# Kernel tuning notes

Measured on AMD Instinct MI355X. Metric: run time of the kernel, lower is better.

## Reference

```python
import jax, jax.numpy as jnp
import numpy as np
from jax import lax

NPOINT = 1024
RADIUS = 0.2
NSAMPLE = 32
BN_EPS = 1e-5


def setup_inputs() -> dict:
    key = jax.random.key(0)
    ks = jax.random.split(key, 8)
    B, N, C = 16, 4096, 6
    xyz = jax.random.uniform(ks[0], (B, N, 3), jnp.float32)
    points = jax.random.normal(ks[1], (B, N, C), jnp.float32)
    dims = [3 + C, 64, 64, 128]
    inp = {"xyz": xyz, "points": points}
    for i in range(3):
        inp[f"W{i}"] = (jax.random.normal(ks[2 + i], (dims[i + 1], dims[i]), jnp.float32)
                         / np.sqrt(dims[i]).astype(np.float32))
        inp[f"b{i}"] = jnp.zeros((dims[i + 1],), jnp.float32)
        inp[f"g{i}"] = jnp.ones((dims[i + 1],), jnp.float32)
        inp[f"bb{i}"] = jnp.zeros((dims[i + 1],), jnp.float32)
    return inp


def _square_distance(a, b):
    # a: (B,S,3), b: (B,N,3) -> (B,S,N) squared euclidean distances
    return (jnp.sum(a * a, -1)[:, :, None]
            - 2.0 * jnp.einsum("bsd,bnd->bsn", a, b)
            + jnp.sum(b * b, -1)[:, None, :])


def _farthest_point_sample(xyz, npoint):
    # xyz: (B,N,3) -> (B,npoint) int32 indices. Deterministic init at index 0.
    B, N, _ = xyz.shape
    bidx = jnp.arange(B)

    def step(carry, _):
        dist, farthest = carry  # (B,N), (B,)
        centroid = xyz[bidx, farthest]  # (B,3)
        d = jnp.sum((xyz - centroid[:, None, :]) ** 2, -1)  # (B,N)
        dist = jnp.minimum(dist, d)
        nxt = jnp.argmax(dist, axis=-1).astype(jnp.int32)
        return (dist, nxt), farthest

    init = (jnp.full((B, N), 1e10, jnp.float32), jnp.zeros((B,), jnp.int32))
    _, idx = lax.scan(step, init, None, length=npoint)
    return idx.T  # (B, npoint)


def _ball_query(radius, nsample, xyz, new_xyz):
    # xyz: (B,N,3), new_xyz: (B,S,3) -> (B,S,nsample) int32 indices
    B, N, _ = xyz.shape
    S = new_xyz.shape[1]
    sqr = _square_distance(new_xyz, xyz)  # (B,S,N)
    group_idx = jnp.broadcast_to(jnp.arange(N, dtype=jnp.int32), (B, S, N))
    group_idx = jnp.where(sqr > radius * radius, N, group_idx)
    group_idx = jnp.sort(group_idx, axis=-1)[:, :, :nsample]
    first = group_idx[:, :, :1]
    return jnp.where(group_idx == N, first, group_idx)


def _index_points(points, idx):
    # points: (B,N,C), idx: (B,...) -> (B,...,C)
    return jax.vmap(lambda p, i: p[i])(points, idx)


def _mlp_bn_relu(x, params):
    # x: (..., Cin); BatchNorm1d in training mode over all flattened rows.
    shape = x.shape
    h = x.reshape(-1, shape[-1])
    for (W, b, g, bb) in params:
        h = h @ W.T + b
        mu = jnp.mean(h, axis=0)
        var = jnp.mean((h - mu) ** 2, axis=0)  # biased var (torch BN forward)
        h = (h - mu) * lax.rsqrt(var + BN_EPS) * g + bb
        h = jax.nn.relu(h)
    return h.reshape(*shape[:-1], -1)


def reference(xyz, points, W0, b0, g0, bb0, W1, b1, g1, bb1, W2, b2, g2, bb2):
    params = [(W0, b0, g0, bb0), (W1, b1, g1, bb1), (W2, b2, g2, bb2)]
    fps_idx = _farthest_point_sample(xyz, NPOINT)          # (B,S)
    new_xyz = _index_points(xyz, fps_idx)                  # (B,S,3)
    idx = _ball_query(RADIUS, NSAMPLE, xyz, new_xyz)       # (B,S,K)
    grouped_xyz = _index_points(xyz, idx) - new_xyz[:, :, None, :]  # (B,S,K,3)
    grouped_pts = _index_points(points, idx)               # (B,S,K,C)
    combined = jnp.concatenate([grouped_xyz, grouped_pts], axis=-1)
    out = _mlp_bn_relu(combined, params)                   # (B,S,K,128)
    new_points = jnp.max(out, axis=2)                      # (B,S,128)
    return new_xyz, new_points
```

## Files before the change

kernel.cpp:

```cpp
#include <hip/hip_runtime.h>

typedef unsigned short u16;
typedef unsigned long long u64;
typedef float f32x2 __attribute__((ext_vector_type(2)));

#define NN 4096
#define SS 1024
#define NSAMP 32
#define NGRP 16384
#define ROWS 524288
#define BN_EPS_F 1e-5f
#define INV_ROWS (1.0f/524288.0f)

__device__ __forceinline__ f32x2 pk_fma_sv(f32x2 w, f32x2 x, f32x2 c){
    f32x2 d; asm("v_pk_fma_f32 %0, %1, %2, %3" : "=v"(d) : "s"(w), "v"(x), "v"(c)); return d;
}

#define FPS_DPP_STEP(CTRL)                                                              \
    {   int hs = __builtin_amdgcn_update_dpp((int)(bk >> 32), (int)(bk >> 32),          \
                                             CTRL, 0xf, 0xf, false);                    \
        int ls = __builtin_amdgcn_update_dpp((int)bk, (int)bk, CTRL, 0xf, 0xf, false);  \
        u64 o = ((u64)(unsigned int)hs << 32) | (unsigned int)ls;                       \
        bk = bk > o ? bk : o; }

__global__ __launch_bounds__(256, 1) void fps_kernel(const float* __restrict__ xyz,
                                                     float* __restrict__ out,
                                                     float* __restrict__ stats){
    __shared__ float xs[NN], ys[NN], zs[NN];
    __shared__ u64 red[2][4];
    const int b = blockIdx.x;
    const int tid = threadIdx.x;
    if (b == 0){ stats[tid] = 0.0f; stats[tid + 256] = 0.0f; }
    const float* xb = xyz + (size_t)b * NN * 3;
    float px[16], py[16], pz[16], dreg[16];
    unsigned int inv[16];
    #pragma unroll
    for (int p = 0; p < 16; ++p){
        int i = tid + p * 256;
        float x = xb[i*3+0], y = xb[i*3+1], z = xb[i*3+2];
        px[p] = x; py[p] = y; pz[p] = z;
        xs[i] = x; ys[i] = y; zs[i] = z;
        dreg[p] = 1e10f;
        inv[p] = (unsigned int)(NN - 1 - i);
    }
    int cur = 0;
    __syncthreads();
    if (tid == 0){
        float* of = out + (size_t)b * SS * 3;
        of[0] = xs[0]; of[1] = ys[0]; of[2] = zs[0];
    }
    const int wave = tid >> 6, lane = tid & 63;
    for (int it = 1; it < SS; ++it){
        float cx = xs[cur], cy = ys[cur], cz = zs[cur];
        u64 t[16];
        #pragma unroll
        for (int p = 0; p < 16; ++p){
            float dx = __fsub_rn(px[p], cx);
            float dy = __fsub_rn(py[p], cy);
            float dz = __fsub_rn(pz[p], cz);
            float dd = __fadd_rn(__fadd_rn(__fmul_rn(dx,dx), __fmul_rn(dy,dy)),
                                 __fmul_rn(dz,dz));
            dreg[p] = fminf(dreg[p], dd);
            t[p] = ((u64)__float_as_uint(dreg[p]) << 32) | inv[p];
        }
        #pragma unroll
        for (int s = 8; s >= 1; s >>= 1)
            #pragma unroll
            for (int i2 = 0; i2 < s; ++i2)
                if (t[i2 + s] > t[i2]) t[i2] = t[i2 + s];
        u64 bk = t[0];
        FPS_DPP_STEP(0x111)
        FPS_DPP_STEP(0x112)
        FPS_DPP_STEP(0x114)
        FPS_DPP_STEP(0x118)
        FPS_DPP_STEP(0x142)
        FPS_DPP_STEP(0x143)
        unsigned int wh = (unsigned int)__builtin_amdgcn_readlane((int)(bk >> 32), 63);
        unsigned int wl = (unsigned int)__builtin_amdgcn_readlane((int)bk, 63);
        if (lane == 0) red[it & 1][wave] = ((u64)wh << 32) | wl;
        __syncthreads();
        u64 r0 = red[it & 1][0], r1 = red[it & 1][1];
        u64 r2 = red[it & 1][2], r3 = red[it & 1][3];
        u64 a01 = r0 > r1 ? r0 : r1;
        u64 a23 = r2 > r3 ? r2 : r3;
        u64 m0  = a01 > a23 ? a01 : a23;
        cur = (NN - 1 - (int)(m0 & 0xffffffffu)) & (NN - 1);
        if (tid == 0){
            float* of = out + ((size_t)b * SS + it) * 3;
            of[0] = xs[cur]; of[1] = ys[cur]; of[2] = zs[cur];
        }
    }
}

__global__ __launch_bounds__(256) void ballq_kernel(const float* __restrict__ xyz,
                                                    const float* __restrict__ outc,
                                                    u16* __restrict__ gidx){
    const int g = (blockIdx.x << 2) + (threadIdx.x >> 6);
    const int lane = threadIdx.x & 63;
    const int b = g >> 10;
    const float rr = 0.04f;
    const float* c = outc + (size_t)g * 3;
    float cx = c[0], cy = c[1], cz = c[2];
    float sa = __fadd_rn(__fadd_rn(__fmul_rn(cx,cx), __fmul_rn(cy,cy)), __fmul_rn(cz,cz));
    const float* xb = xyz + (size_t)b * NN * 3;
    u16* outp = gidx + (size_t)g * NSAMP;
    int count = 0, first = -1;
    const u64 below = (1ull << lane) - 1ull;
    for (int base = 0; base < NN && count < NSAMP; base += 512){
        u64 masks[8];
        #pragma unroll
        for (int u = 0; u < 8; ++u){
            int n = base + u * 64 + lane;
            float x = xb[n*3+0], y = xb[n*3+1], z = xb[n*3+2];
            float sb = __fadd_rn(__fadd_rn(__fmul_rn(x,x), __fmul_rn(y,y)), __fmul_rn(z,z));
            float dt = __fadd_rn(__fadd_rn(__fmul_rn(cx,x), __fmul_rn(cy,y)), __fmul_rn(cz,z));
            float sq = __fadd_rn(__fsub_rn(sa, __fmul_rn(2.0f, dt)), sb);
            masks[u] = __ballot(!(sq > rr));
        }
        #pragma unroll
        for (int u = 0; u < 8; ++u){
            u64 m = masks[u];
            bool w = (m >> lane) & 1ull;
            int pos = __popcll(m & below);
            if (w && (count + pos) < NSAMP) outp[count + pos] = (u16)(base + u * 64 + lane);
            if (first < 0 && m != 0ull) first = base + u * 64 + (__ffsll((long long)m) - 1);
            count += __popcll(m);
        }
    }
    for (int j = count + lane; j < NSAMP; j += 64) outp[j] = (u16)first;
}

__device__ __forceinline__ void gather_row(const float* __restrict__ xyz, const float* __restrict__ pts,
                                           const float* __restrict__ outc, const u16* __restrict__ gidx,
                                           int row, float* x){
    int g = row >> 5;
    int b = row >> 15;
    int i = gidx[row];
    const float* cc = outc + (size_t)g * 3;
    const float* xp = xyz + ((size_t)b * NN + i) * 3;
    const float* pp = pts + ((size_t)b * NN + i) * 6;
    x[0] = __fsub_rn(xp[0], cc[0]);
    x[1] = __fsub_rn(xp[1], cc[1]);
    x[2] = __fsub_rn(xp[2], cc[2]);
    #pragma unroll
    for (int k = 0; k < 6; ++k) x[3+k] = pp[k];
}

__device__ __forceinline__ void bn_coef(const float* sums, const float* ssqs,
                                        const float* g, const float* bbv, int ch,
                                        float* sc, float* sh){
    float mu = sums[ch] * INV_ROWS;
    float var = fmaf(-mu, mu, ssqs[ch] * INV_ROWS);
    var = fmaxf(var, 0.0f);
    float is = rsqrtf(var + BN_EPS_F);
    float s = is * g[ch];
    sc[ch] = s;
    sh[ch] = fmaf(-mu, s, bbv[ch]);
}

__global__ __launch_bounds__(256, 1) void stats1_kernel(const float* __restrict__ xyz, const float* __restrict__ pts,
                                                        const float* __restrict__ outc, const u16* __restrict__ gidx,
                                                        const float* __restrict__ W0f, const float* __restrict__ b0f,
                                                        float* __restrict__ stats){
    __shared__ float tr[256 * 65];
    __shared__ float accs[4][64], accq[4][64];
    const int row = blockIdx.x * 256 + threadIdx.x;
    float x[9];
    gather_row(xyz, pts, outc, gidx, row, x);
    #pragma unroll
    for (int j = 0; j < 64; ++j){
        float acc = b0f[j];
        #pragma unroll
        for (int k = 0; k < 9; ++k) acc = fmaf(x[k], W0f[j*9+k], acc);
        tr[threadIdx.x * 65 + j] = acc;
    }
    __syncthreads();
    const int ch = threadIdx.x & 63, qq = threadIdx.x >> 6;
    float s = 0.f, q = 0.f;
    for (int r = 0; r < 64; ++r){
        float v = tr[(qq * 64 + r) * 65 + ch];
        s += v; q = fmaf(v, v, q);
    }
    accs[qq][ch] = s; accq[qq][ch] = q;
    __syncthreads();
    if (threadIdx.x < 64){
        int c = threadIdx.x;
        atomicAdd(&stats[c], (accs[0][c] + accs[1][c]) + (accs[2][c] + accs[3][c]));
    } else if (threadIdx.x < 128){
        int c = threadIdx.x - 64;
        atomicAdd(&stats[64 + c], (accq[0][c] + accq[1][c]) + (accq[2][c] + accq[3][c]));
    }
}

__global__ __launch_bounds__(256, 1) void stats2_kernel(const float* __restrict__ xyz, const float* __restrict__ pts,
                                                        const float* __restrict__ outc, const u16* __restrict__ gidx,
                                                        const float* __restrict__ W0f, const float* __restrict__ b0f,
                                                        const float* __restrict__ W1f, const float* __restrict__ b1f,
                                                        const float* __restrict__ g0, const float* __restrict__ bb0,
                                                        float* __restrict__ stats){
    __shared__ float sc1[64], sh1[64];
    __shared__ float tr[256 * 65];
    __shared__ float accs[4][64], accq[4][64];
    if (threadIdx.x < 64) bn_coef(stats + 0, stats + 64, g0, bb0, threadIdx.x, sc1, sh1);
    __syncthreads();
    const int row = blockIdx.x * 256 + threadIdx.x;
    float x[9];
    gather_row(xyz, pts, outc, gidx, row, x);
    f32x2 x2p[32];
    #pragma unroll
    for (int j = 0; j < 64; ++j){
        float acc = b0f[j];
        #pragma unroll
        for (int k = 0; k < 9; ++k) acc = fmaf(x[k], W0f[j*9+k], acc);
        float v = fmaxf(fmaf(acc, sc1[j], sh1[j]), 0.f);
        if (j & 1) x2p[j >> 1].y = v; else x2p[j >> 1].x = v;
    }
    for (int ch = 0; ch < 64; ++ch){
        const f32x2* wp = (const f32x2*)(W1f + ch * 64);
        f32x2 A; A.x = b1f[ch]; A.y = 0.f;
        f32x2 B; B.x = 0.f;     B.y = 0.f;
        #pragma unroll
        for (int k2 = 0; k2 < 32; k2 += 2){
            A = pk_fma_sv(wp[k2],     x2p[k2],     A);
            B = pk_fma_sv(wp[k2 + 1], x2p[k2 + 1], B);
        }
        tr[threadIdx.x * 65 + ch] = (A.x + A.y) + (B.x + B.y);
    }
    __syncthreads();
    const int ch = threadIdx.x & 63, qq = threadIdx.x >> 6;
    float s = 0.f, q = 0.f;
    for (int r = 0; r < 64; ++r){
        float v = tr[(qq * 64 + r) * 65 + ch];
        s += v; q = fmaf(v, v, q);
    }
    accs[qq][ch] = s; accq[qq][ch] = q;
    __syncthreads();
    if (threadIdx.x < 64){
        int c = threadIdx.x;
        atomicAdd(&stats[128 + c], (accs[0][c] + accs[1][c]) + (accs[2][c] + accs[3][c]));
    } else if (threadIdx.x < 128){
        int c = threadIdx.x - 64;
        atomicAdd(&stats[192 + c], (accq[0][c] + accq[1][c]) + (accq[2][c] + accq[3][c]));
    }
}

__global__ __launch_bounds__(256, 1) void stats3_kernel(const float* __restrict__ xyz, const float* __restrict__ pts,
                                                        const float* __restrict__ outc, const u16* __restrict__ gidx,
                                                        const float* __restrict__ W0f, const float* __restrict__ b0f,
                                                        const float* __restrict__ W1f, const float* __restrict__ b1f,
                                                        const float* __restrict__ W2f, const float* __restrict__ b2f,
                                                        const float* __restrict__ g0, const float* __restrict__ bb0,
                                                        const float* __restrict__ g1, const float* __restrict__ bb1,
                                                        float* __restrict__ stats,
                                                        float* __restrict__ pmax, float* __restrict__ pmin){
    __shared__ float sc1[64], sh1[64], sc2[64], sh2[64];
    __shared__ float tr[256 * 65];
    __shared__ float accs[4][64], accq[4][64];
    if (threadIdx.x < 64){
        bn_coef(stats + 0,   stats + 64,  g0, bb0, threadIdx.x, sc1, sh1);
        bn_coef(stats + 128, stats + 192, g1, bb1, threadIdx.x, sc2, sh2);
    }
    __syncthreads();
    const int row = blockIdx.x * 256 + threadIdx.x;
    float x[9];
    gather_row(xyz, pts, outc, gidx, row, x);
    f32x2 x2p[32];
    #pragma unroll
    for (int j = 0; j < 64; ++j){
        float acc = b0f[j];
        #pragma unroll
        for (int k = 0; k < 9; ++k) acc = fmaf(x[k], W0f[j*9+k], acc);
        float v = fmaxf(fmaf(acc, sc1[j], sh1[j]), 0.f);
        if (j & 1) x2p[j >> 1].y = v; else x2p[j >> 1].x = v;
    }
    #pragma unroll
    for (int j = 0; j < 64; ++j){
        const f32x2* wp = (const f32x2*)(W1f + j * 64);
        f32x2 A; A.x = b1f[j]; A.y = 0.f;
        f32x2 B; B.x = 0.f;    B.y = 0.f;
        #pragma unroll
        for (int k2 = 0; k2 < 32; k2 += 2){
            A = pk_fma_sv(wp[k2],     x2p[k2],     A);
            B = pk_fma_sv(wp[k2 + 1], x2p[k2 + 1], B);
        }
        tr[threadIdx.x * 65 + j] = fmaxf(fmaf((A.x + A.y) + (B.x + B.y), sc2[j], sh2[j]), 0.f);
    }
    asm volatile("" ::: "memory");
    f32x2 x3p[32];
    #pragma unroll
    for (int j = 0; j < 32; ++j){
        x3p[j].x = tr[threadIdx.x * 65 + 2*j];
        x3p[j].y = tr[threadIdx.x * 65 + 2*j + 1];
    }
    const int ch = threadIdx.x & 63, qq = threadIdx.x >> 6;
    for (int half = 0; half < 2; ++half){
        for (int c64 = 0; c64 < 64; ++c64){
            int c = half * 64 + c64;
            const f32x2* wp = (const f32x2*)(W2f + c * 64);
            f32x2 A; A.x = b2f[c]; A.y = 0.f;
            f32x2 B; B.x = 0.f;    B.y = 0.f;
            #pragma unroll
            for (int k2 = 0; k2 < 32; k2 += 2){
                A = pk_fma_sv(wp[k2],     x3p[k2],     A);
                B = pk_fma_sv(wp[k2 + 1], x3p[k2 + 1], B);
            }
            tr[threadIdx.x * 65 + c64] = (A.x + A.y) + (B.x + B.y);
        }
        __syncthreads();
        float s = 0.f, q = 0.f;
        float mxA = -1e30f, mnA = 1e30f, mxB = -1e30f, mnB = 1e30f;
        for (int r = 0; r < 32; ++r){
            float v = tr[(qq * 64 + r) * 65 + ch];
            s += v; q = fmaf(v, v, q);
            mxA = fmaxf(mxA, v); mnA = fminf(mnA, v);
        }
        for (int r = 32; r < 64; ++r){
            float v = tr[(qq * 64 + r) * 65 + ch];
            s += v; q = fmaf(v, v, q);
            mxB = fmaxf(mxB, v); mnB = fminf(mnB, v);
        }
        int c = half * 64 + ch;
        int gA = blockIdx.x * 8 + 2 * qq;
        pmax[(size_t)gA * 128 + c] = mxA;
        pmin[(size_t)gA * 128 + c] = mnA;
        pmax[(size_t)(gA + 1) * 128 + c] = mxB;
        pmin[(size_t)(gA + 1) * 128 + c] = mnB;
        accs[qq][ch] = s; accq[qq][ch] = q;
        __syncthreads();
        if (threadIdx.x < 64){
            int cc = half * 64 + threadIdx.x;
            atomicAdd(&stats[256 + cc], (accs[0][threadIdx.x] + accs[1][threadIdx.x])
                                      + (accs[2][threadIdx.x] + accs[3][threadIdx.x]));
        } else if (threadIdx.x < 128){
            int t = threadIdx.x - 64;
            int cc = half * 64 + t;
            atomicAdd(&stats[384 + cc], (accq[0][t] + accq[1][t]) + (accq[2][t] + accq[3][t]));
        }
        __syncthreads();
    }
}

__global__ __launch_bounds__(256) void pool_kernel(const float* __restrict__ stats,
                                                   const float* __restrict__ g2, const float* __restrict__ bb2,
                                                   const float* __restrict__ pmax, const float* __restrict__ pmin,
                                                   float* __restrict__ out){
    __shared__ float sc[128], sh[128];
    if (threadIdx.x < 128) bn_coef(stats + 256, stats + 384, g2, bb2, threadIdx.x, sc, sh);
    __syncthreads();
    int o = blockIdx.x * 256 + threadIdx.x;
    int ch = o & 127;
    float a = fmaf(pmax[o], sc[ch], sh[ch]);
    float b = fmaf(pmin[o], sc[ch], sh[ch]);
    out[NGRP * 3 + o] = fmaxf(fmaxf(a, b), 0.0f);
}

extern "C" void kernel_launch(void* const* d_in, const int* in_sizes, int n_in,
                              void* d_out, int out_size, void* d_ws, size_t ws_size,
                              hipStream_t stream){
    const float* xyz = (const float*)d_in[0];
    const float* pts = (const float*)d_in[1];
    const float* W0  = (const float*)d_in[2];
    const float* b0  = (const float*)d_in[3];
    const float* g0  = (const float*)d_in[4];
    const float* bb0 = (const float*)d_in[5];
    const float* W1  = (const float*)d_in[6];
    const float* b1  = (const float*)d_in[7];
    const float* g1  = (const float*)d_in[8];
    const float* bb1 = (const float*)d_in[9];
    const float* W2  = (const float*)d_in[10];
    const float* b2  = (const float*)d_in[11];
    const float* g2  = (const float*)d_in[12];
    const float* bb2 = (const float*)d_in[13];
    float* out = (float*)d_out;

    if (ws_size < 17827840u) return;
    char*  ws    = (char*)d_ws;
    float* stats = (float*)ws;
    u16*   gidx  = (u16*)  (ws + 2048);
    float* pmax  = (float*)(ws + 1050624);
    float* pmin  = (float*)(ws + 9439232);

    fps_kernel  <<<16, 256, 0, stream>>>(xyz, out, stats);
    ballq_kernel<<<NGRP/4, 256, 0, stream>>>(xyz, out, gidx);
    stats1_kernel<<<ROWS/256, 256, 0, stream>>>(xyz, pts, out, gidx, W0, b0, stats);
    stats2_kernel<<<ROWS/256, 256, 0, stream>>>(xyz, pts, out, gidx, W0, b0, W1, b1, g0, bb0, stats);
    stats3_kernel<<<ROWS/256, 256, 0, stream>>>(xyz, pts, out, gidx, W0, b0, W1, b1, W2, b2,
                                                g0, bb0, g1, bb1, stats, pmax, pmin);
    pool_kernel <<<NGRP*128/256, 256, 0, stream>>>(stats, g2, bb2, pmax, pmin, out);
}
```

Measured before the change: 1.235 ms.

## Halve shared transpose buffer to 32 columns to allow four blocks per CU

The three BN-statistics kernels now stage 32 channels at a time in a 256x33 shared transpose buffer instead of all 64 in a 256x65 buffer, doing the reduction in two or four passes. Launch bounds go from one to four blocks per CU. This cuts LDS use per block from about 66KB to about 34KB and caps register use, so more waves can hide gather and ALU latency. The cost is extra barriers and reduction passes, more atomics per block, and a risk of register spills under the tighter launch bound, since stats3 keeps 64 f32x2 activation registers live.

```diff
diff --git a/kernel.cpp b/kernel.cpp
--- a/kernel.cpp
+++ b/kernel.cpp
@@ -158,49 +158,59 @@
     sh[ch] = fmaf(-mu, s, bbv[ch]);
 }
 
-__global__ __launch_bounds__(256, 1) void stats1_kernel(const float* __restrict__ xyz, const float* __restrict__ pts,
+
+__global__ __launch_bounds__(256, 4) void stats1_kernel(const float* __restrict__ xyz, const float* __restrict__ pts,
                                                         const float* __restrict__ outc, const u16* __restrict__ gidx,
                                                         const float* __restrict__ W0f, const float* __restrict__ b0f,
                                                         float* __restrict__ stats){
-    __shared__ float tr[256 * 65];
-    __shared__ float accs[4][64], accq[4][64];
+    __shared__ float tr[256 * 33];
+    __shared__ float accs[8][32], accq[8][32];
     const int row = blockIdx.x * 256 + threadIdx.x;
     float x[9];
     gather_row(xyz, pts, outc, gidx, row, x);
-    #pragma unroll
-    for (int j = 0; j < 64; ++j){
-        float acc = b0f[j];
-        #pragma unroll
-        for (int k = 0; k < 9; ++k) acc = fmaf(x[k], W0f[j*9+k], acc);
-        tr[threadIdx.x * 65 + j] = acc;
-    }
-    __syncthreads();
-    const int ch = threadIdx.x & 63, qq = threadIdx.x >> 6;
-    float s = 0.f, q = 0.f;
-    for (int r = 0; r < 64; ++r){
-        float v = tr[(qq * 64 + r) * 65 + ch];
-        s += v; q = fmaf(v, v, q);
-    }
-    accs[qq][ch] = s; accq[qq][ch] = q;
-    __syncthreads();
-    if (threadIdx.x < 64){
-        int c = threadIdx.x;
-        atomicAdd(&stats[c], (accs[0][c] + accs[1][c]) + (accs[2][c] + accs[3][c]));
-    } else if (threadIdx.x < 128){
-        int c = threadIdx.x - 64;
-        atomicAdd(&stats[64 + c], (accq[0][c] + accq[1][c]) + (accq[2][c] + accq[3][c]));
-    }
-}
-
-__global__ __launch_bounds__(256, 1) void stats2_kernel(const float* __restrict__ xyz, const float* __restrict__ pts,
+    const int ch = threadIdx.x & 31, oc = threadIdx.x >> 5;
+    #pragma unroll
+    for (int h2 = 0; h2 < 2; ++h2){
+        #pragma unroll
+        for (int j = 0; j < 32; ++j){
+            int jj = h2 * 32 + j;
+            float acc = b0f[jj];
+            #pragma unroll
+            for (int k = 0; k < 9; ++k) acc = fmaf(x[k], W0f[jj*9+k], acc);
+            tr[threadIdx.x * 33 + j] = acc;
+        }
+        __syncthreads();
+        float s = 0.f, q = 0.f;
+        for (int r = 0; r < 32; ++r){
+            float v = tr[(oc * 32 + r) * 33 + ch];
+            s += v; q = fmaf(v, v, q);
+        }
+        accs[oc][ch] = s; accq[oc][ch] = q;
+        __syncthreads();
+        if (threadIdx.x < 32){
+            int t = threadIdx.x;
+            float t0 = (accs[0][t] + accs[1][t]) + (accs[2][t] + accs[3][t]);
+            float t1 = (accs[4][t] + accs[5][t]) + (accs[6][t] + accs[7][t]);
+            atomicAdd(&stats[h2 * 32 + t], t0 + t1);
+        } else if (threadIdx.x < 64){
+            int t = threadIdx.x - 32;
+            float t0 = (accq[0][t] + accq[1][t]) + (accq[2][t] + accq[3][t]);
+            float t1 = (accq[4][t] + accq[5][t]) + (accq[6][t] + accq[7][t]);
+            atomicAdd(&stats[64 + h2 * 32 + t], t0 + t1);
+        }
+        __syncthreads();
+    }
+}
+
+__global__ __launch_bounds__(256, 4) void stats2_kernel(const float* __restrict__ xyz, const float* __restrict__ pts,
                                                         const float* __restrict__ outc, const u16* __restrict__ gidx,
                                                         const float* __restrict__ W0f, const float* __restrict__ b0f,
                                                         const float* __restrict__ W1f, const float* __restrict__ b1f,
                                                         const float* __restrict__ g0, const float* __restrict__ bb0,
                                                         float* __restrict__ stats){
     __shared__ float sc1[64], sh1[64];
-    __shared__ float tr[256 * 65];
-    __shared__ float accs[4][64], accq[4][64];
+    __shared__ float tr[256 * 33];
+    __shared__ float accs[8][32], accq[8][32];
     if (threadIdx.x < 64) bn_coef(stats + 0, stats + 64, g0, bb0, threadIdx.x, sc1, sh1);
     __syncthreads();
     const int row = blockIdx.x * 256 + threadIdx.x;
@@ -215,36 +225,45 @@
         float v = fmaxf(fmaf(acc, sc1[j], sh1[j]), 0.f);
         if (j & 1) x2p[j >> 1].y = v; else x2p[j >> 1].x = v;
     }
-    for (int ch = 0; ch < 64; ++ch){
-        const f32x2* wp = (const f32x2*)(W1f + ch * 64);
-        f32x2 A; A.x = b1f[ch]; A.y = 0.f;
-        f32x2 B; B.x = 0.f;     B.y = 0.f;
-        #pragma unroll
-        for (int k2 = 0; k2 < 32; k2 += 2){
-            A = pk_fma_sv(wp[k2],     x2p[k2],     A);
-            B = pk_fma_sv(wp[k2 + 1], x2p[k2 + 1], B);
-        }
-        tr[threadIdx.x * 65 + ch] = (A.x + A.y) + (B.x + B.y);
-    }
-    __syncthreads();
-    const int ch = threadIdx.x & 63, qq = threadIdx.x >> 6;
-    float s = 0.f, q = 0.f;
-    for (int r = 0; r < 64; ++r){
-        float v = tr[(qq * 64 + r) * 65 + ch];
-        s += v; q = fmaf(v, v, q);
-    }
-    accs[qq][ch] = s; accq[qq][ch] = q;
-    __syncthreads();
-    if (threadIdx.x < 64){
-        int c = threadIdx.x;
-        atomicAdd(&stats[128 + c], (accs[0][c] + accs[1][c]) + (accs[2][c] + accs[3][c]));
-    } else if (threadIdx.x < 128){
-        int c = threadIdx.x - 64;
-        atomicAdd(&stats[192 + c], (accq[0][c] + accq[1][c]) + (accq[2][c] + accq[3][c]));
-    }
-}
-
-__global__ __launch_bounds__(256, 1) void stats3_kernel(const float* __restrict__ xyz, const float* __restrict__ pts,
+    const int ch = threadIdx.x & 31, oc = threadIdx.x >> 5;
+    #pragma unroll
+    for (int h2 = 0; h2 < 2; ++h2){
+        for (int chh = 0; chh < 32; ++chh){
+            int c = h2 * 32 + chh;
+            const f32x2* wp = (const f32x2*)(W1f + c * 64);
+            f32x2 A; A.x = b1f[c]; A.y = 0.f;
+            f32x2 B; B.x = 0.f;    B.y = 0.f;
+            #pragma unroll
+            for (int k2 = 0; k2 < 32; k2 += 2){
+                A = pk_fma_sv(wp[k2],     x2p[k2],     A);
+                B = pk_fma_sv(wp[k2 + 1], x2p[k2 + 1], B);
+            }
+            tr[threadIdx.x * 33 + chh] = (A.x + A.y) + (B.x + B.y);
+        }
+        __syncthreads();
+        float s = 0.f, q = 0.f;
+        for (int r = 0; r < 32; ++r){
+            float v = tr[(oc * 32 + r) * 33 + ch];
+            s += v; q = fmaf(v, v, q);
+        }
+        accs[oc][ch] = s; accq[oc][ch] = q;
+        __syncthreads();
+        if (threadIdx.x < 32){
+            int t = threadIdx.x;
+            float t0 = (accs[0][t] + accs[1][t]) + (accs[2][t] + accs[3][t]);
+            float t1 = (accs[4][t] + accs[5][t]) + (accs[6][t] + accs[7][t]);
+            atomicAdd(&stats[128 + h2 * 32 + t], t0 + t1);
+        } else if (threadIdx.x < 64){
+            int t = threadIdx.x - 32;
+            float t0 = (accq[0][t] + accq[1][t]) + (accq[2][t] + accq[3][t]);
+            float t1 = (accq[4][t] + accq[5][t]) + (accq[6][t] + accq[7][t]);
+            atomicAdd(&stats[192 + h2 * 32 + t], t0 + t1);
+        }
+        __syncthreads();
+    }
+}
+
+__global__ __launch_bounds__(256, 4) void stats3_kernel(const float* __restrict__ xyz, const float* __restrict__ pts,
                                                         const float* __restrict__ outc, const u16* __restrict__ gidx,
                                                         const float* __restrict__ W0f, const float* __restrict__ b0f,
                                                         const float* __restrict__ W1f, const float* __restrict__ b1f,
@@ -254,8 +273,8 @@
                                                         float* __restrict__ stats,
                                                         float* __restrict__ pmax, float* __restrict__ pmin){
     __shared__ float sc1[64], sh1[64], sc2[64], sh2[64];
-    __shared__ float tr[256 * 65];
-    __shared__ float accs[4][64], accq[4][64];
+    __shared__ float tr[256 * 33];
+    __shared__ float accs[8][32], accq[8][32];
     if (threadIdx.x < 64){
         bn_coef(stats + 0,   stats + 64,  g0, bb0, threadIdx.x, sc1, sh1);
         bn_coef(stats + 128, stats + 192, g1, bb1, threadIdx.x, sc2, sh2);
@@ -273,8 +292,9 @@
         float v = fmaxf(fmaf(acc, sc1[j], sh1[j]), 0.f);
         if (j & 1) x2p[j >> 1].y = v; else x2p[j >> 1].x = v;
     }
-    #pragma unroll
-    for (int j = 0; j < 64; ++j){
+    f32x2 x3a[16], x3b[16];
+    #pragma unroll
+    for (int j = 0; j < 32; ++j){
         const f32x2* wp = (const f32x2*)(W1f + j * 64);
         f32x2 A; A.x = b1f[j]; A.y = 0.f;
         f32x2 B; B.x = 0.f;    B.y = 0.f;
@@ -283,60 +303,82 @@
             A = pk_fma_sv(wp[k2],     x2p[k2],     A);
             B = pk_fma_sv(wp[k2 + 1], x2p[k2 + 1], B);
         }
-        tr[threadIdx.x * 65 + j] = fmaxf(fmaf((A.x + A.y) + (B.x + B.y), sc2[j], sh2[j]), 0.f);
+        tr[threadIdx.x * 33 + j] = fmaxf(fmaf((A.x + A.y) + (B.x + B.y), sc2[j], sh2[j]), 0.f);
     }
     asm volatile("" ::: "memory");
-    f32x2 x3p[32];
-    #pragma unroll
-    for (int j = 0; j < 32; ++j){
-        x3p[j].x = tr[threadIdx.x * 65 + 2*j];
-        x3p[j].y = tr[threadIdx.x * 65 + 2*j + 1];
-    }
-    const int ch = threadIdx.x & 63, qq = threadIdx.x >> 6;
+    #pragma unroll
+    for (int j = 0; j < 16; ++j){
+        x3a[j].x = tr[threadIdx.x * 33 + 2*j];
+        x3a[j].y = tr[threadIdx.x * 33 + 2*j + 1];
+    }
+    #pragma unroll
+    for (int j = 32; j < 64; ++j){
+        const f32x2* wp = (const f32x2*)(W1f + j * 64);
+        f32x2 A; A.x = b1f[j]; A.y = 0.f;
+        f32x2 B; B.x = 0.f;    B.y = 0.f;
+        #pragma unroll
+        for (int k2 = 0; k2 < 32; k2 += 2){
+            A = pk_fma_sv(wp[k2],     x2p[k2],     A);
+            B = pk_fma_sv(wp[k2 + 1], x2p[k2 + 1], B);
+        }
+        tr[threadIdx.x * 33 + (j - 32)] = fmaxf(fmaf((A.x + A.y) + (B.x + B.y), sc2[j], sh2[j]), 0.f);
+    }
+    asm volatile("" ::: "memory");
+    #pragma unroll
+    for (int j = 0; j < 16; ++j){
+        x3b[j].x = tr[threadIdx.x * 33 + 2*j];
+        x3b[j].y = tr[threadIdx.x * 33 + 2*j + 1];
+    }
+    const int ch = threadIdx.x & 31, oc = threadIdx.x >> 5;
+    #pragma unroll
     for (int half = 0; half < 2; ++half){
-        for (int c64 = 0; c64 < 64; ++c64){
-            int c = half * 64 + c64;
-            const f32x2* wp = (const f32x2*)(W2f + c * 64);
-            f32x2 A; A.x = b2f[c]; A.y = 0.f;
-            f32x2 B; B.x = 0.f;    B.y = 0.f;
-            #pragma unroll
-            for (int k2 = 0; k2 < 32; k2 += 2){
-                A = pk_fma_sv(wp[k2],     x3p[k2],     A);
-                B = pk_fma_sv(wp[k2 + 1], x3p[k2 + 1], B);
+        #pragma unroll
+        for (int h2 = 0; h2 < 2; ++h2){
+            for (int cc = 0; cc < 32; ++cc){
+                int c = half * 64 + h2 * 32 + cc;
+                const f32x2* wp = (const f32x2*)(W2f + c * 64);
+                f32x2 A; A.x = b2f[c]; A.y = 0.f;
+                f32x2 B; B.x = 0.f;    B.y = 0.f;
+                #pragma unroll
+                for (int k2 = 0; k2 < 16; k2 += 2){
+                    A = pk_fma_sv(wp[k2],     x3a[k2],     A);
+                    B = pk_fma_sv(wp[k2 + 1], x3a[k2 + 1], B);
+                }
+                #pragma unroll
+                for (int k2 = 16; k2 < 32; k2 += 2){
+                    A = pk_fma_sv(wp[k2],     x3b[k2 - 16],     A);
+                    B = pk_fma_sv(wp[k2 + 1], x3b[k2 - 15],     B);
+                }
+                tr[threadIdx.x * 33 + cc] = (A.x + A.y) + (B.x + B.y);
             }
-            tr[threadIdx.x * 65 + c64] = (A.x + A.y) + (B.x + B.y);
-        }
-        __syncthreads();
-        float s = 0.f, q = 0.f;
-        float mxA = -1e30f, mnA = 1e30f, mxB = -1e30f, mnB = 1e30f;
-        for (int r = 0; r < 32; ++r){
-            float v = tr[(qq * 64 + r) * 65 + ch];
-            s += v; q = fmaf(v, v, q);
-            mxA = fmaxf(mxA, v); mnA = fminf(mnA, v);
-        }
-        for (int r = 32; r < 64; ++r){
-            float v = tr[(qq * 64 + r) * 65 + ch];
-            s += v; q = fmaf(v, v, q);
-            mxB = fmaxf(mxB, v); mnB = fminf(mnB, v);
-        }
-        int c = half * 64 + ch;
-        int gA = blockIdx.x * 8 + 2 * qq;
-        pmax[(size_t)gA * 128 + c] = mxA;
-        pmin[(size_t)gA * 128 + c] = mnA;
-        pmax[(size_t)(gA + 1) * 128 + c] = mxB;
-        pmin[(size_t)(gA + 1) * 128 + c] = mnB;
-        accs[qq][ch] = s; accq[qq][ch] = q;
-        __syncthreads();
-        if (threadIdx.x < 64){
-            int cc = half * 64 + threadIdx.x;
-            atomicAdd(&stats[256 + cc], (accs[0][threadIdx.x] + accs[1][threadIdx.x])
-                                      + (accs[2][threadIdx.x] + accs[3][threadIdx.x]));
-        } else if (threadIdx.x < 128){
-            int t = threadIdx.x - 64;
-            int cc = half * 64 + t;
-            atomicAdd(&stats[384 + cc], (accq[0][t] + accq[1][t]) + (accq[2][t] + accq[3][t]));
-        }
-        __syncthreads();
+            __syncthreads();
+            float s = 0.f, q = 0.f, mx = -1e30f, mn = 1e30f;
+            for (int r = 0; r < 32; ++r){
+                float v = tr[(oc * 32 + r) * 33 + ch];
+                s += v; q = fmaf(v, v, q);
+                mx = fmaxf(mx, v); mn = fminf(mn, v);
+            }
+            int c = half * 64 + h2 * 32 + ch;
+            int gA = blockIdx.x * 8 + oc;
+            pmax[(size_t)gA * 128 + c] = mx;
+            pmin[(size_t)gA * 128 + c] = mn;
+            accs[oc][ch] = s; accq[oc][ch] = q;
+            __syncthreads();
+            if (threadIdx.x < 32){
+                int t = threadIdx.x;
+                int cc2 = half * 64 + h2 * 32 + t;
+                float t0 = (accs[0][t] + accs[1][t]) + (accs[2][t] + accs[3][t]);
+                float t1 = (accs[4][t] + accs[5][t]) + (accs[6][t] + accs[7][t]);
+                atomicAdd(&stats[256 + cc2], t0 + t1);
+            } else if (threadIdx.x < 64){
+                int t = threadIdx.x - 32;
+                int cc2 = half * 64 + h2 * 32 + t;
+                float t0 = (accq[0][t] + accq[1][t]) + (accq[2][t] + accq[3][t]);
+                float t1 = (accq[4][t] + accq[5][t]) + (accq[6][t] + accq[7][t]);
+                atomicAdd(&stats[384 + cc2], t0 + t1);
+            }
+            __syncthreads();
+        }
     }
 }
 
```

Result: faster. 1.087 ms, median of 2 (-12.0%).
